# Optimization experiments

Measured on AMD Instinct MI355X. Metric: run time of the kernel, lower is better.

## Reference

```python
import jax, jax.numpy as jnp
import numpy as np


def setup_inputs() -> dict:
    key = jax.random.key(0)
    k1, k2, k3 = jax.random.split(key, 3)
    N, C, H, W, K = 64, 128, 64, 64, 64
    x = jax.random.normal(k1, (N, C, H, W), dtype=jnp.float32)
    conv_w = jax.random.normal(k2, (K, C), dtype=jnp.float32) * 0.05
    centroids = jax.random.uniform(k3, (K, C), dtype=jnp.float32)
    return {"x": x, "conv_w": conv_w, "centroids": centroids}


def reference(x, conv_w, centroids):
    # x: [N, C, H, W]; conv_w: [K, C] (1x1 conv, no bias); centroids: [K, C]
    n, c = x.shape[:2]
    x_flat = x.reshape(n, c, -1)                      # [N, C, S]
    # 1x1 conv == per-pixel linear map, then softmax over clusters
    logits = jnp.einsum('kc,ncs->nks', conv_w, x_flat)  # [N, K, S]
    a = jax.nn.softmax(logits, axis=1)                  # softmax over K
    # VLAD: sum_s a[n,k,s] * (x[n,:,s] - centroid[k])
    #     = (a @ x^T) - (sum_s a) * centroid   -- two batched GEMMs, no [N,K,C,S] blowup
    vlad = jnp.einsum('nks,ncs->nkc', a, x_flat) - a.sum(axis=-1)[..., None] * centroids[None]
    # intra-normalization (L2 per cluster), flatten, global L2
    vlad = vlad / jnp.linalg.norm(vlad, axis=2, keepdims=True)
    vlad = vlad.reshape(n, -1)
    vlad = vlad / jnp.linalg.norm(vlad, axis=1, keepdims=True)
    return vlad
```

## Files before the change

kernel.cpp:

```cpp
#include <hip/hip_runtime.h>


#define Nn 64
#define Cc 128
#define Ss 4096
#define Kk 64
#define TS 64
#define CH 8
#define SB (TS*CH)

typedef __attribute__((ext_vector_type(8))) short bf16x8;
typedef __attribute__((ext_vector_type(4))) float f32x4;

__device__ __forceinline__ unsigned short f2bf(float f) {
  unsigned u = __float_as_uint(f);
  u = (u + 0x7FFFu + ((u >> 16) & 1u)) >> 16;
  return (unsigned short)u;
}

#define XSC_STR 136
#define XCS_STR 72
#define AKS_STR 72

__launch_bounds__(256, 2)
__global__ void netvlad_main(const float* __restrict__ x,
                             const float* __restrict__ w,
                             float* __restrict__ vlad,
                             float* __restrict__ asum)
{
  __shared__ __align__(16) unsigned short x_sc[TS][XSC_STR];
  __shared__ __align__(16) unsigned short x_cs[Cc][XCS_STR];
  __shared__ __align__(16) unsigned short a_ks[Kk][AKS_STR];

  const int t   = threadIdx.x;
  const int wv  = t >> 6;
  const int l15 = t & 15;
  const int l4  = (t >> 4) & 3;
  const int n   = blockIdx.y;
  const int sb  = blockIdx.x;
  const size_t xbase = (size_t)n * Cc * Ss;

  bf16x8 wfrag[4][4];
#pragma unroll
  for (int mt = 0; mt < 4; ++mt) {
#pragma unroll
    for (int q = 0; q < 4; ++q) {
      const float* wp = w + (16*mt + l15) * Cc + 32*q + 8*l4;
      float4 a = *(const float4*)wp;
      float4 b = *(const float4*)(wp + 4);
      bf16x8 f;
      f[0] = (short)f2bf(a.x); f[1] = (short)f2bf(a.y);
      f[2] = (short)f2bf(a.z); f[3] = (short)f2bf(a.w);
      f[4] = (short)f2bf(b.x); f[5] = (short)f2bf(b.y);
      f[6] = (short)f2bf(b.z); f[7] = (short)f2bf(b.w);
      wfrag[mt][q] = f;
    }
  }

  f32x4 acc3[4][2];
#pragma unroll
  for (int mt = 0; mt < 4; ++mt)
#pragma unroll
    for (int tc = 0; tc < 2; ++tc) acc3[mt][tc] = (f32x4){0.f,0.f,0.f,0.f};
  float asum_reg[4][4];
#pragma unroll
  for (int mt = 0; mt < 4; ++mt)
#pragma unroll
    for (int r = 0; r < 4; ++r) asum_reg[mt][r] = 0.f;

  for (int ch = 0; ch < CH; ++ch) {
    const int s0 = sb * SB + ch * TS;

    {
      const int s4 = 4 * (t & 15);
      const int cb = t >> 4;
#pragma unroll
      for (int it = 0; it < 8; ++it) {
        const int c = cb + 16 * it;
        float4 v = *(const float4*)(x + xbase + (size_t)c * Ss + s0 + s4);
        unsigned p0 = (unsigned)f2bf(v.x) | ((unsigned)f2bf(v.y) << 16);
        unsigned p1 = (unsigned)f2bf(v.z) | ((unsigned)f2bf(v.w) << 16);
        unsigned short* dst = &x_cs[c][s4];
        *(int2*)dst = make_int2((int)p0, (int)p1);
      }
    }
    __syncthreads();

    {
      const int s = t & 63;
#pragma unroll
      for (int j = 0; j < 4; ++j) {
        const int c8 = 8 * wv + 32 * j;
        unsigned short h[8];
#pragma unroll
        for (int i = 0; i < 8; ++i) {
          const int i2 = (i + 2 * wv) & 7;
          h[i2] = x_cs[c8 + i2][s];
        }
        unsigned p0 = (unsigned)h[0] | ((unsigned)h[1] << 16);
        unsigned p1 = (unsigned)h[2] | ((unsigned)h[3] << 16);
        unsigned p2 = (unsigned)h[4] | ((unsigned)h[5] << 16);
        unsigned p3 = (unsigned)h[6] | ((unsigned)h[7] << 16);
        *(int4*)&x_sc[s][c8] = make_int4((int)p0, (int)p1, (int)p2, (int)p3);
      }
    }
    __syncthreads();

    f32x4 acc1[4];
#pragma unroll
    for (int mt = 0; mt < 4; ++mt) acc1[mt] = (f32x4){0.f,0.f,0.f,0.f};
#pragma unroll
    for (int q = 0; q < 4; ++q) {
      bf16x8 bfr = *(bf16x8*)&x_sc[16*wv + l15][32*q + 8*l4];
#pragma unroll
      for (int mt = 0; mt < 4; ++mt)
        acc1[mt] = __builtin_amdgcn_mfma_f32_16x16x32_bf16(wfrag[mt][q], bfr, acc1[mt], 0, 0, 0);
    }

    float e[4][4];
    float cs = 0.f;
#pragma unroll
    for (int mt = 0; mt < 4; ++mt)
#pragma unroll
      for (int r = 0; r < 4; ++r) {
        float ev = __expf(acc1[mt][r]);
        e[mt][r] = ev;
        cs += ev;
      }
    cs += __shfl_xor(cs, 16, 64);
    cs += __shfl_xor(cs, 32, 64);
    const float inv = 1.0f / cs;
#pragma unroll
    for (int mt = 0; mt < 4; ++mt)
#pragma unroll
      for (int r = 0; r < 4; ++r) {
        float an = e[mt][r] * inv;
        asum_reg[mt][r] += an;
        a_ks[16*mt + 4*l4 + r][16*wv + l15] = f2bf(an);
      }
    __syncthreads();

#pragma unroll
    for (int q2 = 0; q2 < 2; ++q2) {
      bf16x8 afr[4];
#pragma unroll
      for (int mt = 0; mt < 4; ++mt)
        afr[mt] = *(bf16x8*)&a_ks[16*mt + l15][32*q2 + 8*l4];
#pragma unroll
      for (int tc = 0; tc < 2; ++tc) {
        bf16x8 bfr = *(bf16x8*)&x_cs[32*wv + 16*tc + l15][32*q2 + 8*l4];
#pragma unroll
        for (int mt = 0; mt < 4; ++mt)
          acc3[mt][tc] = __builtin_amdgcn_mfma_f32_16x16x32_bf16(afr[mt], bfr, acc3[mt][tc], 0, 0, 0);
      }
    }
    __syncthreads();
  }

#pragma unroll
  for (int mt = 0; mt < 4; ++mt) {
#pragma unroll
    for (int r = 0; r < 4; ++r) {
      float v = asum_reg[mt][r];
      v += __shfl_xor(v, 1, 64);
      v += __shfl_xor(v, 2, 64);
      v += __shfl_xor(v, 4, 64);
      v += __shfl_xor(v, 8, 64);
      if (l15 == 0) atomicAdd(&asum[n * Kk + 16*mt + 4*l4 + r], v);
    }
  }
#pragma unroll
  for (int mt = 0; mt < 4; ++mt)
#pragma unroll
    for (int tc = 0; tc < 2; ++tc)
#pragma unroll
      for (int r = 0; r < 4; ++r) {
        const int k = 16*mt + 4*l4 + r;
        const int c = 32*wv + 16*tc + l15;
        atomicAdd(&vlad[((size_t)n * Kk + k) * Cc + c], acc3[mt][tc][r]);
      }
}

__global__ void netvlad_epilogue(const float* __restrict__ vlad,
                                 const float* __restrict__ asum,
                                 const float* __restrict__ cent,
                                 float* __restrict__ out)
{
  const int n = blockIdx.x;
  const int t = threadIdx.x;
  const int k = t >> 2;
  const int cq = t & 3;

  __shared__ float red[Kk][4];

  const float ak = asum[n * Kk + k];
  float4 v[8];
  float ss = 0.f;
#pragma unroll
  for (int i = 0; i < 8; ++i) {
    const int c = 4*cq + 16*i;
    float4 xv = *(const float4*)(vlad + ((size_t)n * Kk + k) * Cc + c);
    float4 cv = *(const float4*)(cent + k * Cc + c);
    float4 r;
    r.x = xv.x - ak * cv.x;
    r.y = xv.y - ak * cv.y;
    r.z = xv.z - ak * cv.z;
    r.w = xv.w - ak * cv.w;
    v[i] = r;
    ss += r.x*r.x + r.y*r.y + r.z*r.z + r.w*r.w;
  }
  red[k][cq] = ss;
  __syncthreads();
  const float s4 = red[k][0] + red[k][1] + red[k][2] + red[k][3];
  const float rn = rsqrtf(s4) * 0.125f;
#pragma unroll
  for (int i = 0; i < 8; ++i) {
    const int c = 4*cq + 16*i;
    float4 r = v[i];
    r.x *= rn; r.y *= rn; r.z *= rn; r.w *= rn;
    *(float4*)(out + (size_t)n * (Kk * Cc) + k * Cc + c) = r;
  }
}

extern "C" void kernel_launch(void* const* d_in, const int* in_sizes, int n_in,
                              void* d_out, int out_size, void* d_ws, size_t ws_size,
                              hipStream_t stream)
{
  const float* x    = (const float*)d_in[0];
  const float* w    = (const float*)d_in[1];
  const float* cent = (const float*)d_in[2];
  float* out  = (float*)d_out;
  float* vlad = (float*)d_ws;
  float* asum = vlad + (size_t)Nn * Kk * Cc;

  const size_t zbytes = ((size_t)Nn * Kk * Cc + (size_t)Nn * Kk) * sizeof(float);
  hipMemsetAsync(d_ws, 0, zbytes, stream);

  netvlad_main<<<dim3(Ss / SB, Nn), 256, 0, stream>>>(x, w, vlad, asum);
  netvlad_epilogue<<<Nn, 256, 0, stream>>>(vlad, asum, cent, out);
}
```

Baseline: 237.3 us.

## Prefetch next x chunk into registers, drop a barrier, and widen the epilogue grid

The main kernel now loads the next 64-pixel chunk of x into registers while the current chunk is converted and processed, so global load latency overlaps with the GEMMs and softmax. The x transpose is remapped so each wave writes only the x_sc rows it later reads, which removes one __syncthreads per chunk. Chunks per block drop from 8 to 4 and launch bounds go from 2 to 3 blocks per CU, giving more blocks and higher occupancy at the cost of twice as many atomics into the workspace. The epilogue is spread over 4x more blocks and uses a shuffle reduction instead of shared memory.

```diff
diff --git a/kernel.cpp b/kernel.cpp
--- a/kernel.cpp
+++ b/kernel.cpp
@@ -6,23 +6,23 @@
 #define Ss 4096
 #define Kk 64
 #define TS 64
-#define CH 8
+#define CH 4
 #define SB (TS*CH)
 
 typedef __attribute__((ext_vector_type(8))) short bf16x8;
 typedef __attribute__((ext_vector_type(4))) float f32x4;
 
-__device__ __forceinline__ unsigned short f2bf(float f) {
+__device__ __forceinline__ unsigned f2bf(float f) {
   unsigned u = __float_as_uint(f);
   u = (u + 0x7FFFu + ((u >> 16) & 1u)) >> 16;
-  return (unsigned short)u;
+  return u;
 }
 
 #define XSC_STR 136
 #define XCS_STR 72
 #define AKS_STR 72
 
-__launch_bounds__(256, 2)
+__launch_bounds__(256, 3)
 __global__ void netvlad_main(const float* __restrict__ x,
                              const float* __restrict__ w,
                              float* __restrict__ vlad,
@@ -68,43 +68,52 @@
 #pragma unroll
     for (int r = 0; r < 4; ++r) asum_reg[mt][r] = 0.f;
 
+  const int s4 = 4 * l15;
+  const int cb = t >> 4;
+  float4 v[8];
+  {
+    const float* px = x + xbase + (size_t)cb * Ss + sb * SB + s4;
+#pragma unroll
+    for (int it = 0; it < 8; ++it)
+      v[it] = *(const float4*)(px + (size_t)(16 * it) * Ss);
+  }
+
   for (int ch = 0; ch < CH; ++ch) {
     const int s0 = sb * SB + ch * TS;
 
+#pragma unroll
+    for (int it = 0; it < 8; ++it) {
+      float4 vv = v[it];
+      unsigned p0 = f2bf(vv.x) | (f2bf(vv.y) << 16);
+      unsigned p1 = f2bf(vv.z) | (f2bf(vv.w) << 16);
+      *(int2*)&x_cs[cb + 16*it][s4] = make_int2((int)p0, (int)p1);
+    }
+    if (ch + 1 < CH) {
+      const float* px = x + xbase + (size_t)cb * Ss + s0 + TS + s4;
+#pragma unroll
+      for (int it = 0; it < 8; ++it)
+        v[it] = *(const float4*)(px + (size_t)(16 * it) * Ss);
+    }
+    __syncthreads();
+
     {
-      const int s4 = 4 * (t & 15);
-      const int cb = t >> 4;
-#pragma unroll
-      for (int it = 0; it < 8; ++it) {
-        const int c = cb + 16 * it;
-        float4 v = *(const float4*)(x + xbase + (size_t)c * Ss + s0 + s4);
-        unsigned p0 = (unsigned)f2bf(v.x) | ((unsigned)f2bf(v.y) << 16);
-        unsigned p1 = (unsigned)f2bf(v.z) | ((unsigned)f2bf(v.w) << 16);
-        unsigned short* dst = &x_cs[c][s4];
-        *(int2*)dst = make_int2((int)p0, (int)p1);
-      }
-    }
-    __syncthreads();
-
-    {
-      const int s = t & 63;
+      const int srow = 16*wv + l15;
 #pragma unroll
       for (int j = 0; j < 4; ++j) {
-        const int c8 = 8 * wv + 32 * j;
+        const int c8 = 32*j + 8*l4;
         unsigned short h[8];
 #pragma unroll
         for (int i = 0; i < 8; ++i) {
-          const int i2 = (i + 2 * wv) & 7;
-          h[i2] = x_cs[c8 + i2][s];
+          const int i2 = (i + 2*l4) & 7;
+          h[i2] = x_cs[c8 + i2][srow];
         }
         unsigned p0 = (unsigned)h[0] | ((unsigned)h[1] << 16);
         unsigned p1 = (unsigned)h[2] | ((unsigned)h[3] << 16);
         unsigned p2 = (unsigned)h[4] | ((unsigned)h[5] << 16);
         unsigned p3 = (unsigned)h[6] | ((unsigned)h[7] << 16);
-        *(int4*)&x_sc[s][c8] = make_int4((int)p0, (int)p1, (int)p2, (int)p3);
-      }
-    }
-    __syncthreads();
+        *(int4*)&x_sc[srow][c8] = make_int4((int)p0, (int)p1, (int)p2, (int)p3);
+      }
+    }
 
     f32x4 acc1[4];
 #pragma unroll
@@ -136,7 +145,7 @@
       for (int r = 0; r < 4; ++r) {
         float an = e[mt][r] * inv;
         asum_reg[mt][r] += an;
-        a_ks[16*mt + 4*l4 + r][16*wv + l15] = f2bf(an);
+        a_ks[16*mt + 4*l4 + r][16*wv + l15] = (unsigned short)f2bf(an);
       }
     __syncthreads();
 
@@ -161,12 +170,12 @@
   for (int mt = 0; mt < 4; ++mt) {
 #pragma unroll
     for (int r = 0; r < 4; ++r) {
-      float v = asum_reg[mt][r];
-      v += __shfl_xor(v, 1, 64);
-      v += __shfl_xor(v, 2, 64);
-      v += __shfl_xor(v, 4, 64);
-      v += __shfl_xor(v, 8, 64);
-      if (l15 == 0) atomicAdd(&asum[n * Kk + 16*mt + 4*l4 + r], v);
+      float vv = asum_reg[mt][r];
+      vv += __shfl_xor(vv, 1, 64);
+      vv += __shfl_xor(vv, 2, 64);
+      vv += __shfl_xor(vv, 4, 64);
+      vv += __shfl_xor(vv, 8, 64);
+      if (l15 == 0) atomicAdd(&asum[n * Kk + 16*mt + 4*l4 + r], vv);
     }
   }
 #pragma unroll
@@ -186,40 +195,33 @@
                                  const float* __restrict__ cent,
                                  float* __restrict__ out)
 {
-  const int n = blockIdx.x;
-  const int t = threadIdx.x;
-  const int k = t >> 2;
-  const int cq = t & 3;
-
-  __shared__ float red[Kk][4];
+  const int n  = blockIdx.x;
+  const int k  = 16*blockIdx.y + (threadIdx.x >> 4);
+  const int cq = threadIdx.x & 15;
 
   const float ak = asum[n * Kk + k];
-  float4 v[8];
-  float ss = 0.f;
-#pragma unroll
-  for (int i = 0; i < 8; ++i) {
-    const int c = 4*cq + 16*i;
-    float4 xv = *(const float4*)(vlad + ((size_t)n * Kk + k) * Cc + c);
-    float4 cv = *(const float4*)(cent + k * Cc + c);
-    float4 r;
-    r.x = xv.x - ak * cv.x;
-    r.y = xv.y - ak * cv.y;
-    r.z = xv.z - ak * cv.z;
-    r.w = xv.w - ak * cv.w;
-    v[i] = r;
-    ss += r.x*r.x + r.y*r.y + r.z*r.z + r.w*r.w;
-  }
-  red[k][cq] = ss;
-  __syncthreads();
-  const float s4 = red[k][0] + red[k][1] + red[k][2] + red[k][3];
-  const float rn = rsqrtf(s4) * 0.125f;
-#pragma unroll
-  for (int i = 0; i < 8; ++i) {
-    const int c = 4*cq + 16*i;
-    float4 r = v[i];
-    r.x *= rn; r.y *= rn; r.z *= rn; r.w *= rn;
-    *(float4*)(out + (size_t)n * (Kk * Cc) + k * Cc + c) = r;
-  }
+  const size_t base = ((size_t)n * Kk + k) * Cc + 8*cq;
+  const size_t cbse = (size_t)k * Cc + 8*cq;
+
+  float4 x0 = *(const float4*)(vlad + base);
+  float4 x1 = *(const float4*)(vlad + base + 4);
+  float4 c0 = *(const float4*)(cent + cbse);
+  float4 c1 = *(const float4*)(cent + cbse + 4);
+  float4 r0, r1;
+  r0.x = x0.x - ak*c0.x; r0.y = x0.y - ak*c0.y; r0.z = x0.z - ak*c0.z; r0.w = x0.w - ak*c0.w;
+  r1.x = x1.x - ak*c1.x; r1.y = x1.y - ak*c1.y; r1.z = x1.z - ak*c1.z; r1.w = x1.w - ak*c1.w;
+  float ss = r0.x*r0.x + r0.y*r0.y + r0.z*r0.z + r0.w*r0.w
+           + r1.x*r1.x + r1.y*r1.y + r1.z*r1.z + r1.w*r1.w;
+  ss += __shfl_xor(ss, 1, 64);
+  ss += __shfl_xor(ss, 2, 64);
+  ss += __shfl_xor(ss, 4, 64);
+  ss += __shfl_xor(ss, 8, 64);
+  const float rn = rsqrtf(ss) * 0.125f;
+  r0.x *= rn; r0.y *= rn; r0.z *= rn; r0.w *= rn;
+  r1.x *= rn; r1.y *= rn; r1.z *= rn; r1.w *= rn;
+  float* op = out + (size_t)n * (Kk * Cc) + (size_t)k * Cc + 8*cq;
+  *(float4*)op = r0;
+  *(float4*)(op + 4) = r1;
 }
 
 extern "C" void kernel_launch(void* const* d_in, const int* in_sizes, int n_in,
@@ -237,5 +239,5 @@
   hipMemsetAsync(d_ws, 0, zbytes, stream);
 
   netvlad_main<<<dim3(Ss / SB, Nn), 256, 0, stream>>>(x, w, vlad, asum);
-  netvlad_epilogue<<<Nn, 256, 0, stream>>>(vlad, asum, cent, out);
-}
+  netvlad_epilogue<<<dim3(Nn, 4), 256, 0, stream>>>(vlad, asum, cent, out);
+}
```

New measurement: 267.8 us. 1.13x slower.
